# Kernel optimization log

Hardware: AMD Instinct MI355X
Metric: run time of the kernel (lower is better)

The kernel has to match this reference:

```python
import jax, jax.numpy as jnp
from jax import lax
import numpy as np

B, S, D, H = 256, 2048, 16, 128
HH = H // 2  # head hidden = 64


def _p(key, shape, scale=0.05):
    return scale * jax.random.normal(key, shape, dtype=jnp.float32)


def setup_inputs() -> dict:
    key = jax.random.key(0)
    ks = jax.random.split(key, 12)
    return {
        "x": jax.random.normal(ks[0], (B, S, D), dtype=jnp.float32),
        # LSTM layer 0 (PyTorch gate order: i, f, g, o along the 4H axis)
        "W_ih0": _p(ks[1], (4 * H, D)),
        "W_hh0": _p(ks[2], (4 * H, H)),
        "b_ih0": jnp.zeros((4 * H,), jnp.float32),
        "b_hh0": jnp.zeros((4 * H,), jnp.float32),
        # LSTM layer 1
        "W_ih1": _p(ks[3], (4 * H, H)),
        "W_hh1": _p(ks[4], (4 * H, H)),
        "b_ih1": jnp.zeros((4 * H,), jnp.float32),
        "b_hh1": jnp.zeros((4 * H,), jnp.float32),
        # return head: Linear(H, H//2) -> LeakyReLU -> Linear(H//2, 1)
        "Wr1": _p(ks[5], (HH, H)), "br1": jnp.zeros((HH,), jnp.float32),
        "Wr2": _p(ks[6], (1, HH)), "br2": jnp.zeros((1,), jnp.float32),
        # vol head: Linear -> LeakyReLU -> Linear -> Softplus
        "Wv1": _p(ks[7], (HH, H)), "bv1": jnp.zeros((HH,), jnp.float32),
        "Wv2": _p(ks[8], (1, HH)), "bv2": jnp.zeros((1,), jnp.float32),
    }


def _lstm_layer(x, W_ih, W_hh, b_ih, b_hh):
    # x: (B, S, Din) -> hs: (B, S, H); PyTorch gate order i, f, g, o
    b, s, _ = x.shape
    h_dim = W_hh.shape[1]
    xg = jnp.einsum('bsd,gd->bsg', x, W_ih) + (b_ih + b_hh)  # (B, S, 4H)

    def step(carry, xg_t):
        h, c = carry
        g = xg_t + h @ W_hh.T
        i, f, gc, o = jnp.split(g, 4, axis=-1)
        i = jax.nn.sigmoid(i)
        f = jax.nn.sigmoid(f)
        gc = jnp.tanh(gc)
        o = jax.nn.sigmoid(o)
        c = f * c + i * gc
        h = o * jnp.tanh(c)
        return (h, c), h

    h0 = jnp.zeros((b, h_dim), x.dtype)
    (hN, cN), hs = lax.scan(step, (h0, jnp.zeros_like(h0)), jnp.swapaxes(xg, 0, 1))
    return jnp.swapaxes(hs, 0, 1), hN, cN


def reference(x, W_ih0, W_hh0, b_ih0, b_hh0, W_ih1, W_hh1, b_ih1, b_hh1,
              Wr1, br1, Wr2, br2, Wv1, bv1, Wv2, bv2):
    h1, hN0, cN0 = _lstm_layer(x, W_ih0, W_hh0, b_ih0, b_hh0)
    # inter-layer dropout is inactive at inference (eval mode)
    h2, hN1, cN1 = _lstm_layer(h1, W_ih1, W_hh1, b_ih1, b_hh1)
    # return head
    r = jax.nn.leaky_relu(jnp.einsum('bsh,kh->bsk', h2, Wr1) + br1)
    returns = jnp.einsum('bsk,ok->bso', r, Wr2) + br2
    # volatility head
    v = jax.nn.leaky_relu(jnp.einsum('bsh,kh->bsk', h2, Wv1) + bv1)
    volatility = jax.nn.softplus(jnp.einsum('bsk,ok->bso', v, Wv2) + bv2)
    hidden_h = jnp.stack([hN0, hN1], axis=0)  # (num_layers, B, H)
    hidden_c = jnp.stack([cN0, cN1], axis=0)
    return returns, volatility, hidden_h, hidden_c
```

## Files before the change

kernel.cpp:

```cpp
#include <hip/hip_runtime.h>
#include <hip/hip_bf16.h>

#define B_ 256
#define S_ 2048
#define D_ 16
#define H_ 128

typedef unsigned int u32;
typedef unsigned short u16;
typedef _Float16 h2t __attribute__((ext_vector_type(2)));

#define RET0 ((size_t)0)
#define VOL0 ((size_t)524288)
#define HH0  ((size_t)1048576)
#define HC0  ((size_t)1114112)

__device__ __forceinline__ float fdot2(u32 a, u32 b, float c) {
    return __builtin_amdgcn_fdot2(__builtin_bit_cast(h2t, a),
                                  __builtin_bit_cast(h2t, b), c, false);
}
__device__ __forceinline__ u32 packh2(float a, float b) {
    h2t h; h[0] = (_Float16)a; h[1] = (_Float16)b;
    return __builtin_bit_cast(u32, h);
}
__device__ __forceinline__ float sigm(float x) {
    return __builtin_amdgcn_rcpf(1.f + __builtin_amdgcn_exp2f(-1.44269504f * x));
}
__device__ __forceinline__ float tanh_(float x) {
    return 2.f * __builtin_amdgcn_rcpf(1.f + __builtin_amdgcn_exp2f(-2.88539008f * x)) - 1.f;
}
__device__ __forceinline__ float softplus_(float x) {
    if (x > 20.f) return x;
    const float e = __builtin_amdgcn_exp2f(1.44269504f * x);
    return 0.69314718f * __builtin_amdgcn_logf(1.f + e);
}

__global__ __launch_bounds__(512) void k_l0(
    const float* __restrict__ x, const float* __restrict__ Wih,
    const float* __restrict__ Whh, const float* __restrict__ bih,
    const float* __restrict__ bhh, u32* __restrict__ h1out,
    float* __restrict__ out)
{
    __shared__ float xs[512 * 16];
    __shared__ float gates[4][128];
    __shared__ float hf[128];
    __shared__ u32 och[64 * 64];

    const int tid = threadIdx.x, b = blockIdx.x;
    const int g = tid >> 7, m = tid & 127, row = g * 128 + m;

    float wx[16], wh[128];
#pragma unroll
    for (int j = 0; j < 16; ++j) wx[j] = Wih[row * 16 + j];
#pragma unroll
    for (int j = 0; j < 128; ++j) wh[j] = Whh[row * 128 + j];
    const float bs = bih[row] + bhh[row];

    float c = 0.f;
    if (tid < 128) hf[tid] = 0.f;
    __syncthreads();

    const float* xb = x + (size_t)b * S_ * D_;
    for (int t = 0; t < S_; ++t) {
        if ((t & 511) == 0) {
            for (int i = tid; i < 2048; i += 512) {
                const float4 v = *(const float4*)(xb + (size_t)t * 16 + i * 4);
                *(float4*)(&xs[i * 4]) = v;
            }
            __syncthreads();
        }
        float a = bs;
        const float* xt = &xs[(t & 511) * 16];
#pragma unroll
        for (int j = 0; j < 16; ++j) a += wx[j] * xt[j];
#pragma unroll
        for (int j = 0; j < 128; ++j) a += wh[j] * hf[j];
        gates[g][m] = a;
        __syncthreads();
        if (tid < 128) {
            const float ig = sigm(gates[0][tid]);
            const float fg = sigm(gates[1][tid]);
            const float gc = tanh_(gates[2][tid]);
            const float og = sigm(gates[3][tid]);
            c = fg * c + ig * gc;
            const float h = og * tanh_(c);
            hf[tid] = h;
            if (t == S_ - 1) {
                out[HH0 + (size_t)b * H_ + tid] = h;
                out[HC0 + (size_t)b * H_ + tid] = c;
            }
        }
        __syncthreads();
        if (tid < 64) och[(t & 63) * 64 + tid] = packh2(hf[2 * tid], hf[2 * tid + 1]);
        if ((t & 63) == 63) {
            __syncthreads();
            u32* dst = h1out + ((size_t)b * S_ + (t - 63)) * 64;
            *(uint4*)(dst + tid * 8)     = *(const uint4*)(&och[tid * 8]);
            *(uint4*)(dst + tid * 8 + 4) = *(const uint4*)(&och[tid * 8 + 4]);
        }
        __syncthreads();
    }
}

__global__ __launch_bounds__(512) void k_l1(
    u32* __restrict__ hws,
    const float* __restrict__ Wih, const float* __restrict__ Whh,
    const float* __restrict__ bih, const float* __restrict__ bhh,
    float* __restrict__ out)
{
    __shared__ u32 h1w[128 * 64];
    __shared__ float gates[4][128];
    __shared__ u32 hp[64];
    __shared__ u32 och[64 * 64];

    const int tid = threadIdx.x, b = blockIdx.x;
    const int g = tid >> 7, m = tid & 127, row = g * 128 + m;

    u32 wi[64], wh[64];
#pragma unroll
    for (int j = 0; j < 64; ++j) {
        const float2 a = *(const float2*)(Wih + row * 128 + 2 * j);
        const float2 cc = *(const float2*)(Whh + row * 128 + 2 * j);
        wi[j] = packh2(a.x, a.y);
        wh[j] = packh2(cc.x, cc.y);
    }
    const float bs = bih[row] + bhh[row];

    float c = 0.f;
    if (tid < 64) hp[tid] = 0u;
    __syncthreads();

    u32* hb = hws + (size_t)b * S_ * 64;
    for (int t = 0; t < S_; ++t) {
        if ((t & 127) == 0) {
            for (int i = tid; i < 2048; i += 512)
                *(uint4*)(&h1w[i * 4]) = *(const uint4*)(hb + (size_t)t * 64 + i * 4);
            __syncthreads();
        }
        float a = bs;
        const u32* h1t = &h1w[(t & 127) * 64];
#pragma unroll
        for (int j = 0; j < 64; ++j) a = fdot2(h1t[j], wi[j], a);
#pragma unroll
        for (int j = 0; j < 64; ++j) a = fdot2(hp[j], wh[j], a);
        gates[g][m] = a;
        __syncthreads();
        if (tid < 128) {
            const float ig = sigm(gates[0][tid]);
            const float fg = sigm(gates[1][tid]);
            const float gc = tanh_(gates[2][tid]);
            const float og = sigm(gates[3][tid]);
            c = fg * c + ig * gc;
            const float h = og * tanh_(c);
            ((u16*)hp)[tid] = __builtin_bit_cast(unsigned short, (_Float16)h);
            if (t == S_ - 1) {
                out[HH0 + 32768 + (size_t)b * H_ + tid] = h;
                out[HC0 + 32768 + (size_t)b * H_ + tid] = c;
            }
        }
        __syncthreads();
        if (tid < 64) och[(t & 63) * 64 + tid] = hp[tid];
        if ((t & 63) == 63) {
            __syncthreads();
            u32* dst = hb + (size_t)(t - 63) * 64;
            *(uint4*)(dst + tid * 8)     = *(const uint4*)(&och[tid * 8]);
            *(uint4*)(dst + tid * 8 + 4) = *(const uint4*)(&och[tid * 8 + 4]);
        }
        __syncthreads();
    }
}

__global__ __launch_bounds__(256) void k_heads(
    const u32* __restrict__ h2p,
    const float* __restrict__ Wr1, const float* __restrict__ br1,
    const float* __restrict__ Wr2, const float* __restrict__ br2,
    const float* __restrict__ Wv1, const float* __restrict__ bv1,
    const float* __restrict__ Wv2, const float* __restrict__ bv2,
    float* __restrict__ out)
{
    __shared__ u32 wr[64 * 64], wv[64 * 64];
    __shared__ float w2r[64], w2v[64], b1r[64], b1v[64];

    const int tid = threadIdx.x;
    for (int i = tid; i < 4096; i += 256) {
        wr[i] = packh2(Wr1[2 * i], Wr1[2 * i + 1]);
        wv[i] = packh2(Wv1[2 * i], Wv1[2 * i + 1]);
    }
    if (tid < 64) {
        w2r[tid] = Wr2[tid]; w2v[tid] = Wv2[tid];
        b1r[tid] = br1[tid]; b1v[tid] = bv1[tid];
    }
    __syncthreads();

    const size_t bs = (size_t)blockIdx.x * 256 + tid;
    u32 hq[64];
    const u32* src = h2p + bs * 64;
#pragma unroll
    for (int j4 = 0; j4 < 16; ++j4) {
        const uint4 v = *(const uint4*)(src + j4 * 4);
        hq[j4 * 4] = v.x; hq[j4 * 4 + 1] = v.y; hq[j4 * 4 + 2] = v.z; hq[j4 * 4 + 3] = v.w;
    }
    float ret = br2[0], vol = bv2[0];
    for (int k = 0; k < 64; ++k) {
        float r = b1r[k], v = b1v[k];
#pragma unroll
        for (int j = 0; j < 64; ++j) r = fdot2(hq[j], wr[k * 64 + j], r);
#pragma unroll
        for (int j = 0; j < 64; ++j) v = fdot2(hq[j], wv[k * 64 + j], v);
        r = r > 0.f ? r : 0.01f * r;
        v = v > 0.f ? v : 0.01f * v;
        ret += r * w2r[k];
        vol += v * w2v[k];
    }
    out[RET0 + bs] = ret;
    out[VOL0 + bs] = softplus_(vol);
}

extern "C" void kernel_launch(void* const* d_in, const int* in_sizes, int n_in,
                              void* d_out, int out_size, void* d_ws, size_t ws_size,
                              hipStream_t stream) {
    (void)in_sizes; (void)n_in; (void)out_size; (void)ws_size;
    const float* x    = (const float*)d_in[0];
    const float* Wih0 = (const float*)d_in[1];
    const float* Whh0 = (const float*)d_in[2];
    const float* bih0 = (const float*)d_in[3];
    const float* bhh0 = (const float*)d_in[4];
    const float* Wih1 = (const float*)d_in[5];
    const float* Whh1 = (const float*)d_in[6];
    const float* bih1 = (const float*)d_in[7];
    const float* bhh1 = (const float*)d_in[8];
    const float* Wr1  = (const float*)d_in[9];
    const float* br1  = (const float*)d_in[10];
    const float* Wr2  = (const float*)d_in[11];
    const float* br2  = (const float*)d_in[12];
    const float* Wv1  = (const float*)d_in[13];
    const float* bv1  = (const float*)d_in[14];
    const float* Wv2  = (const float*)d_in[15];
    const float* bv2  = (const float*)d_in[16];
    u32* hws = (u32*)d_ws;
    float* out = (float*)d_out;

    k_l0<<<B_, 512, 0, stream>>>(x, Wih0, Whh0, bih0, bhh0, hws, out);
    k_l1<<<B_, 512, 0, stream>>>(hws, Wih1, Whh1, bih1, bhh1, out);
    k_heads<<<2048, 256, 0, stream>>>(hws, Wr1, br1, Wr2, br2, Wv1, bv1, Wv2, bv2, out);
}
```

Baseline: 4.117 ms.

## Fuse both LSTM layers and heads into one wavefront-pipelined kernel

After: 4.916 ms. 19.4% more time.

```diff
diff --git a/kernel.cpp b/kernel.cpp
--- a/kernel.cpp
+++ b/kernel.cpp
@@ -5,6 +5,8 @@
 #define S_ 2048
 #define D_ 16
 #define H_ 128
+#define NT 768
+#define NA 256
 
 typedef unsigned int u32;
 typedef unsigned short u16;
@@ -35,191 +37,250 @@
     return 0.69314718f * __builtin_amdgcn_logf(1.f + e);
 }
 
-__global__ __launch_bounds__(512) void k_l0(
-    const float* __restrict__ x, const float* __restrict__ Wih,
-    const float* __restrict__ Whh, const float* __restrict__ bih,
-    const float* __restrict__ bhh, u32* __restrict__ h1out,
-    float* __restrict__ out)
-{
-    __shared__ float xs[512 * 16];
-    __shared__ float gates[4][128];
-    __shared__ float hf[128];
-    __shared__ u32 och[64 * 64];
-
-    const int tid = threadIdx.x, b = blockIdx.x;
-    const int g = tid >> 7, m = tid & 127, row = g * 128 + m;
-
-    float wx[16], wh[128];
-#pragma unroll
-    for (int j = 0; j < 16; ++j) wx[j] = Wih[row * 16 + j];
-#pragma unroll
-    for (int j = 0; j < 128; ++j) wh[j] = Whh[row * 128 + j];
-    const float bs = bih[row] + bhh[row];
-
-    float c = 0.f;
-    if (tid < 128) hf[tid] = 0.f;
-    __syncthreads();
-
-    const float* xb = x + (size_t)b * S_ * D_;
-    for (int t = 0; t < S_; ++t) {
-        if ((t & 511) == 0) {
-            for (int i = tid; i < 2048; i += 512) {
-                const float4 v = *(const float4*)(xb + (size_t)t * 16 + i * 4);
-                *(float4*)(&xs[i * 4]) = v;
-            }
-            __syncthreads();
-        }
-        float a = bs;
-        const float* xt = &xs[(t & 511) * 16];
-#pragma unroll
-        for (int j = 0; j < 16; ++j) a += wx[j] * xt[j];
-#pragma unroll
-        for (int j = 0; j < 128; ++j) a += wh[j] * hf[j];
-        gates[g][m] = a;
-        __syncthreads();
-        if (tid < 128) {
-            const float ig = sigm(gates[0][tid]);
-            const float fg = sigm(gates[1][tid]);
-            const float gc = tanh_(gates[2][tid]);
-            const float og = sigm(gates[3][tid]);
-            c = fg * c + ig * gc;
-            const float h = og * tanh_(c);
-            hf[tid] = h;
-            if (t == S_ - 1) {
-                out[HH0 + (size_t)b * H_ + tid] = h;
-                out[HC0 + (size_t)b * H_ + tid] = c;
-            }
-        }
-        __syncthreads();
-        if (tid < 64) och[(t & 63) * 64 + tid] = packh2(hf[2 * tid], hf[2 * tid + 1]);
-        if ((t & 63) == 63) {
-            __syncthreads();
-            u32* dst = h1out + ((size_t)b * S_ + (t - 63)) * 64;
-            *(uint4*)(dst + tid * 8)     = *(const uint4*)(&och[tid * 8]);
-            *(uint4*)(dst + tid * 8 + 4) = *(const uint4*)(&och[tid * 8 + 4]);
-        }
-        __syncthreads();
-    }
-}
-
-__global__ __launch_bounds__(512) void k_l1(
-    u32* __restrict__ hws,
-    const float* __restrict__ Wih, const float* __restrict__ Whh,
-    const float* __restrict__ bih, const float* __restrict__ bhh,
-    float* __restrict__ out)
-{
-    __shared__ u32 h1w[128 * 64];
-    __shared__ float gates[4][128];
-    __shared__ u32 hp[64];
-    __shared__ u32 och[64 * 64];
-
-    const int tid = threadIdx.x, b = blockIdx.x;
-    const int g = tid >> 7, m = tid & 127, row = g * 128 + m;
-
-    u32 wi[64], wh[64];
-#pragma unroll
-    for (int j = 0; j < 64; ++j) {
-        const float2 a = *(const float2*)(Wih + row * 128 + 2 * j);
-        const float2 cc = *(const float2*)(Whh + row * 128 + 2 * j);
-        wi[j] = packh2(a.x, a.y);
-        wh[j] = packh2(cc.x, cc.y);
-    }
-    const float bs = bih[row] + bhh[row];
-
-    float c = 0.f;
-    if (tid < 64) hp[tid] = 0u;
-    __syncthreads();
-
-    u32* hb = hws + (size_t)b * S_ * 64;
-    for (int t = 0; t < S_; ++t) {
-        if ((t & 127) == 0) {
-            for (int i = tid; i < 2048; i += 512)
-                *(uint4*)(&h1w[i * 4]) = *(const uint4*)(hb + (size_t)t * 64 + i * 4);
-            __syncthreads();
-        }
-        float a = bs;
-        const u32* h1t = &h1w[(t & 127) * 64];
-#pragma unroll
-        for (int j = 0; j < 64; ++j) a = fdot2(h1t[j], wi[j], a);
-#pragma unroll
-        for (int j = 0; j < 64; ++j) a = fdot2(hp[j], wh[j], a);
-        gates[g][m] = a;
-        __syncthreads();
-        if (tid < 128) {
-            const float ig = sigm(gates[0][tid]);
-            const float fg = sigm(gates[1][tid]);
-            const float gc = tanh_(gates[2][tid]);
-            const float og = sigm(gates[3][tid]);
-            c = fg * c + ig * gc;
-            const float h = og * tanh_(c);
-            ((u16*)hp)[tid] = __builtin_bit_cast(unsigned short, (_Float16)h);
-            if (t == S_ - 1) {
-                out[HH0 + 32768 + (size_t)b * H_ + tid] = h;
-                out[HC0 + 32768 + (size_t)b * H_ + tid] = c;
-            }
-        }
-        __syncthreads();
-        if (tid < 64) och[(t & 63) * 64 + tid] = hp[tid];
-        if ((t & 63) == 63) {
-            __syncthreads();
-            u32* dst = hb + (size_t)(t - 63) * 64;
-            *(uint4*)(dst + tid * 8)     = *(const uint4*)(&och[tid * 8]);
-            *(uint4*)(dst + tid * 8 + 4) = *(const uint4*)(&och[tid * 8 + 4]);
-        }
-        __syncthreads();
-    }
-}
-
-__global__ __launch_bounds__(256) void k_heads(
-    const u32* __restrict__ h2p,
+#define GD4(v, i)                                                              \
+    a0 = fdot2(v, w[i], a0);       a1 = fdot2(v, w[36 + (i)], a1);             \
+    a2 = fdot2(v, w[72 + (i)], a2); a3 = fdot2(v, w[108 + (i)], a3);
+#define GD32(v, i)                                                             \
+    a0 = fdot2(v, w[i], a0);       a1 = fdot2(v, w[32 + (i)], a1);             \
+    a2 = fdot2(v, w[64 + (i)], a2); a3 = fdot2(v, w[96 + (i)], a3);
+
+__global__ __launch_bounds__(NT, 3) void mtl_fused(
+    const float* __restrict__ x,
+    const float* __restrict__ Wih0, const float* __restrict__ Whh0,
+    const float* __restrict__ bih0, const float* __restrict__ bhh0,
+    const float* __restrict__ Wih1, const float* __restrict__ Whh1,
+    const float* __restrict__ bih1, const float* __restrict__ bhh1,
     const float* __restrict__ Wr1, const float* __restrict__ br1,
     const float* __restrict__ Wr2, const float* __restrict__ br2,
     const float* __restrict__ Wv1, const float* __restrict__ bv1,
     const float* __restrict__ Wv2, const float* __restrict__ bv2,
     float* __restrict__ out)
 {
-    __shared__ u32 wr[64 * 64], wv[64 * 64];
-    __shared__ float w2r[64], w2v[64], b1r[64], b1v[64];
+    __shared__ u32 xp2[2][4096];
+    __shared__ u32 h1b[2][64];
+    __shared__ u32 h2b[2][64];
+    __shared__ float redbuf[2][8];
+    __shared__ float rvr[S_];
+    __shared__ float rvv[S_];
 
     const int tid = threadIdx.x;
-    for (int i = tid; i < 4096; i += 256) {
-        wr[i] = packh2(Wr1[2 * i], Wr1[2 * i + 1]);
-        wv[i] = packh2(Wv1[2 * i], Wv1[2 * i + 1]);
+    const int b = blockIdx.x;
+    const bool isA = (tid < NA);
+    const int ma = tid >> 1, k0 = tid & 1;
+    const int tb = tid - NA, mb = tb >> 2, q = tb & 3;
+
+    u32 w[144];
+    float bias[4];
+    float hb1 = 0.f, hw2 = 0.f;
+    const float br2f = br2[0], bv2f = bv2[0];
+
+    if (isA) {
+#pragma unroll
+        for (int g = 0; g < 4; ++g) {
+            const int row = g * H_ + ma;
+            const float4* wxr = (const float4*)(Wih0 + row * D_ + k0 * 8);
+#pragma unroll
+            for (int j4 = 0; j4 < 2; ++j4) {
+                const float4 f = wxr[j4];
+                w[g * 36 + j4 * 2]     = packh2(f.x, f.y);
+                w[g * 36 + j4 * 2 + 1] = packh2(f.z, f.w);
+            }
+            const float4* whr = (const float4*)(Whh0 + row * H_ + k0 * 64);
+#pragma unroll
+            for (int j4 = 0; j4 < 16; ++j4) {
+                const float4 f = whr[j4];
+                w[g * 36 + 4 + j4 * 2] = packh2(f.x, f.y);
+                w[g * 36 + 5 + j4 * 2] = packh2(f.z, f.w);
+            }
+            bias[g] = bih0[row] + bhh0[row];
+        }
+    } else {
+#pragma unroll
+        for (int g = 0; g < 4; ++g) {
+            const int row = g * H_ + mb;
+            const float4* wir = (const float4*)(Wih1 + row * H_ + q * 32);
+            const float4* whr = (const float4*)(Whh1 + row * H_ + q * 32);
+#pragma unroll
+            for (int j4 = 0; j4 < 8; ++j4) {
+                float4 f = wir[j4];
+                w[g * 32 + j4 * 2]      = packh2(f.x, f.y);
+                w[g * 32 + j4 * 2 + 1]  = packh2(f.z, f.w);
+                f = whr[j4];
+                w[g * 32 + 16 + j4 * 2] = packh2(f.x, f.y);
+                w[g * 32 + 17 + j4 * 2] = packh2(f.z, f.w);
+            }
+            bias[g] = bih1[row] + bhh1[row];
+        }
+        const bool isret = (mb < 64);
+        const int hr = isret ? mb : mb - 64;
+        const float* W1 = isret ? Wr1 : Wv1;
+        const float4* whr = (const float4*)(W1 + hr * H_ + q * 32);
+#pragma unroll
+        for (int j4 = 0; j4 < 8; ++j4) {
+            const float4 f = whr[j4];
+            w[128 + j4 * 2]     = packh2(f.x, f.y);
+            w[128 + j4 * 2 + 1] = packh2(f.z, f.w);
+        }
+        hb1 = (isret ? br1 : bv1)[hr];
+        hw2 = (isret ? Wr2 : Wv2)[hr];
+    }
+
+    const float* xrow = x + (size_t)b * S_ * D_;
+    for (int i = tid; i < 2048; i += NT) {
+        const float4 v = *(const float4*)(xrow + i * 4);
+        xp2[0][i * 2]     = packh2(v.x, v.y);
+        xp2[0][i * 2 + 1] = packh2(v.z, v.w);
     }
     if (tid < 64) {
-        w2r[tid] = Wr2[tid]; w2v[tid] = Wv2[tid];
-        b1r[tid] = br1[tid]; b1v[tid] = bv1[tid];
-    }
+        h1b[0][tid] = 0u; h1b[1][tid] = 0u;
+        h2b[0][tid] = 0u; h2b[1][tid] = 0u;
+    }
+    if (tid < 16) ((float*)redbuf)[tid] = 0.f;
+    float c1 = 0.f, c2 = 0.f;
     __syncthreads();
 
-    const size_t bs = (size_t)blockIdx.x * 256 + tid;
-    u32 hq[64];
-    const u32* src = h2p + bs * 64;
-#pragma unroll
-    for (int j4 = 0; j4 < 16; ++j4) {
-        const uint4 v = *(const uint4*)(src + j4 * 4);
-        hq[j4 * 4] = v.x; hq[j4 * 4 + 1] = v.y; hq[j4 * 4 + 2] = v.z; hq[j4 * 4 + 3] = v.w;
-    }
-    float ret = br2[0], vol = bv2[0];
-    for (int k = 0; k < 64; ++k) {
-        float r = b1r[k], v = b1v[k];
-#pragma unroll
-        for (int j = 0; j < 64; ++j) r = fdot2(hq[j], wr[k * 64 + j], r);
-#pragma unroll
-        for (int j = 0; j < 64; ++j) v = fdot2(hq[j], wv[k * 64 + j], v);
-        r = r > 0.f ? r : 0.01f * r;
-        v = v > 0.f ? v : 0.01f * v;
-        ret += r * w2r[k];
-        vol += v * w2v[k];
-    }
-    out[RET0 + bs] = ret;
-    out[VOL0 + bs] = softplus_(vol);
+    for (int t = 0; t <= S_; ++t) {
+        if ((t & 511) == 0 && t < S_ - 512) {
+            const int nw = (t >> 9) + 1;
+            u32* dst = xp2[nw & 1];
+            const float* src = xrow + (size_t)nw * 8192;
+            for (int i = tid; i < 2048; i += NT) {
+                const float4 v = *(const float4*)(src + i * 4);
+                dst[i * 2]     = packh2(v.x, v.y);
+                dst[i * 2 + 1] = packh2(v.z, v.w);
+            }
+        }
+        if (t >= 3 && tid == 0) {
+            const float* rb = redbuf[t & 1];
+            rvr[t - 3] = rb[0] + rb[1] + rb[2] + rb[3] + br2f;
+            rvv[t - 3] = softplus_(rb[4] + rb[5] + rb[6] + rb[7] + bv2f);
+        }
+
+        if (isA) {
+            if (t < S_) {
+                float a0 = 0.f, a1 = 0.f, a2 = 0.f, a3 = 0.f;
+                const uint4 xv = *(const uint4*)(&xp2[(t >> 9) & 1][(t & 511) * 8 + k0 * 4]);
+                GD4(xv.x, 0) GD4(xv.y, 1) GD4(xv.z, 2) GD4(xv.w, 3)
+                const uint4* h4 = (const uint4*)(&h1b[(t + 1) & 1][k0 * 32]);
+#pragma unroll
+                for (int p4 = 0; p4 < 8; ++p4) {
+                    const uint4 v = h4[p4];
+                    GD4(v.x, 4 + p4 * 4) GD4(v.y, 5 + p4 * 4)
+                    GD4(v.z, 6 + p4 * 4) GD4(v.w, 7 + p4 * 4)
+                }
+                a0 += __shfl_xor(a0, 1); a1 += __shfl_xor(a1, 1);
+                a2 += __shfl_xor(a2, 1); a3 += __shfl_xor(a3, 1);
+                float h1val = 0.f;
+                if (k0 == 0) {
+                    const float ig = sigm(a0 + bias[0]);
+                    const float fg = sigm(a1 + bias[1]);
+                    const float gc = tanh_(a2 + bias[2]);
+                    const float og = sigm(a3 + bias[3]);
+                    c1 = fg * c1 + ig * gc;
+                    h1val = og * tanh_(c1);
+                }
+                const float hnb = __shfl_down(h1val, 2);
+                if ((tid & 3) == 0) h1b[t & 1][ma >> 1] = packh2(h1val, hnb);
+                if (t == S_ - 1 && k0 == 0) {
+                    out[HH0 + (size_t)b * H_ + ma] = h1val;
+                    out[HC0 + (size_t)b * H_ + ma] = c1;
+                }
+            }
+        } else {
+            if (t >= 1) {
+                const int u = t - 1;
+                float a0 = 0.f, a1 = 0.f, a2 = 0.f, a3 = 0.f, hacc = 0.f;
+                const uint4* h1v = (const uint4*)(&h1b[u & 1][q * 16]);
+#pragma unroll
+                for (int p4 = 0; p4 < 4; ++p4) {
+                    const uint4 v = h1v[p4];
+                    GD32(v.x, p4 * 4)     GD32(v.y, p4 * 4 + 1)
+                    GD32(v.z, p4 * 4 + 2) GD32(v.w, p4 * 4 + 3)
+                }
+                const uint4* h2v = (const uint4*)(&h2b[t & 1][q * 16]);
+#pragma unroll
+                for (int p4 = 0; p4 < 4; ++p4) {
+                    const uint4 v = h2v[p4];
+                    GD32(v.x, 16 + p4 * 4) GD32(v.y, 17 + p4 * 4)
+                    GD32(v.z, 18 + p4 * 4) GD32(v.w, 19 + p4 * 4)
+                    hacc = fdot2(v.x, w[128 + p4 * 4], hacc);
+                    hacc = fdot2(v.y, w[129 + p4 * 4], hacc);
+                    hacc = fdot2(v.z, w[130 + p4 * 4], hacc);
+                    hacc = fdot2(v.w, w[131 + p4 * 4], hacc);
+                }
+                a0 += __shfl_xor(a0, 1); a0 += __shfl_xor(a0, 2);
+                a1 += __shfl_xor(a1, 1); a1 += __shfl_xor(a1, 2);
+                a2 += __shfl_xor(a2, 1); a2 += __shfl_xor(a2, 2);
+                a3 += __shfl_xor(a3, 1); a3 += __shfl_xor(a3, 2);
+                hacc += __shfl_xor(hacc, 1); hacc += __shfl_xor(hacc, 2);
+                float h2val = 0.f, pc = 0.f;
+                if (q == 0) {
+                    const float ig = sigm(a0 + bias[0]);
+                    const float fg = sigm(a1 + bias[1]);
+                    const float gc = tanh_(a2 + bias[2]);
+                    const float og = sigm(a3 + bias[3]);
+                    c2 = fg * c2 + ig * gc;
+                    h2val = og * tanh_(c2);
+                    float d = hacc + hb1;
+                    d = d > 0.f ? d : 0.01f * d;
+                    pc = d * hw2;
+                }
+                pc += __shfl_xor(pc, 4);  pc += __shfl_xor(pc, 8);
+                pc += __shfl_xor(pc, 16); pc += __shfl_xor(pc, 32);
+                if ((tb & 63) == 0) redbuf[u & 1][tb >> 6] = pc;
+                const float hnb = __shfl_down(h2val, 4);
+                if ((tb & 7) == 0) h2b[u & 1][mb >> 1] = packh2(h2val, hnb);
+                if (u == S_ - 1 && q == 0) {
+                    out[HH0 + 32768 + (size_t)b * H_ + mb] = h2val;
+                    out[HC0 + 32768 + (size_t)b * H_ + mb] = c2;
+                }
+            }
+        }
+        __syncthreads();
+    }
+
+    if (!isA) {
+        float hacc = 0.f;
+        const uint4* h2v = (const uint4*)(&h2b[1][q * 16]);
+#pragma unroll
+        for (int p4 = 0; p4 < 4; ++p4) {
+            const uint4 v = h2v[p4];
+            hacc = fdot2(v.x, w[128 + p4 * 4], hacc);
+            hacc = fdot2(v.y, w[129 + p4 * 4], hacc);
+            hacc = fdot2(v.z, w[130 + p4 * 4], hacc);
+            hacc = fdot2(v.w, w[131 + p4 * 4], hacc);
+        }
+        hacc += __shfl_xor(hacc, 1); hacc += __shfl_xor(hacc, 2);
+        float pc = 0.f;
+        if (q == 0) {
+            float d = hacc + hb1;
+            d = d > 0.f ? d : 0.01f * d;
+            pc = d * hw2;
+        }
+        pc += __shfl_xor(pc, 4);  pc += __shfl_xor(pc, 8);
+        pc += __shfl_xor(pc, 16); pc += __shfl_xor(pc, 32);
+        if ((tb & 63) == 0) redbuf[0][tb >> 6] = pc;
+    }
+    __syncthreads();
+    if (tid == 0) {
+        const float* rb = redbuf[1];
+        rvr[S_ - 2] = rb[0] + rb[1] + rb[2] + rb[3] + br2f;
+        rvv[S_ - 2] = softplus_(rb[4] + rb[5] + rb[6] + rb[7] + bv2f);
+        const float* rc = redbuf[0];
+        rvr[S_ - 1] = rc[0] + rc[1] + rc[2] + rc[3] + br2f;
+        rvv[S_ - 1] = softplus_(rc[4] + rc[5] + rc[6] + rc[7] + bv2f);
+    }
+    __syncthreads();
+    for (int s = tid; s < S_; s += NT) {
+        out[RET0 + (size_t)b * S_ + s] = rvr[s];
+        out[VOL0 + (size_t)b * S_ + s] = rvv[s];
+    }
 }
 
 extern "C" void kernel_launch(void* const* d_in, const int* in_sizes, int n_in,
                               void* d_out, int out_size, void* d_ws, size_t ws_size,
                               hipStream_t stream) {
-    (void)in_sizes; (void)n_in; (void)out_size; (void)ws_size;
+    (void)in_sizes; (void)n_in; (void)out_size; (void)d_ws; (void)ws_size;
     const float* x    = (const float*)d_in[0];
     const float* Wih0 = (const float*)d_in[1];
     const float* Whh0 = (const float*)d_in[2];
@@ -237,10 +298,9 @@
     const float* bv1  = (const float*)d_in[14];
     const float* Wv2  = (const float*)d_in[15];
     const float* bv2  = (const float*)d_in[16];
-    u32* hws = (u32*)d_ws;
     float* out = (float*)d_out;
 
-    k_l0<<<B_, 512, 0, stream>>>(x, Wih0, Whh0, bih0, bhh0, hws, out);
-    k_l1<<<B_, 512, 0, stream>>>(hws, Wih1, Whh1, bih1, bhh1, out);
-    k_heads<<<2048, 256, 0, stream>>>(hws, Wr1, br1, Wr2, br2, Wv1, bv1, Wv2, bv2, out);
-}
+    mtl_fused<<<B_, NT, 0, stream>>>(x, Wih0, Whh0, bih0, bhh0,
+                                     Wih1, Whh1, bih1, bhh1,
+                                     Wr1, br1, Wr2, br2, Wv1, bv1, Wv2, bv2, out);
+}
```
